# Performance work log

Hardware: AMD Instinct MI355X
Metric: run time of the kernel (lower is better)

The kernel has to match this reference:

```python
import jax, jax.numpy as jnp
import numpy as np

N = 65536       # n_nodes
E = 1048576     # n_edges (avg degree 16)
IDX = 256       # index_size
DIN = 512       # gcn_input_size
DH = 512        # gcn_hidden_size
DOUT = 128      # gcn_output_size
S = 256         # sample_size


def gcn_conv(h, W, b, src, dst, n):
    # PyG GCNConv: linear, add self-loops, symmetric deg^-1/2 normalization, scatter-add.
    h = h @ W
    loop = jnp.arange(n)
    s = jnp.concatenate([src, loop])
    d = jnp.concatenate([dst, loop])
    deg = jax.ops.segment_sum(jnp.ones(s.shape[0], h.dtype), d, num_segments=n)
    inv_sqrt = jax.lax.rsqrt(deg)  # deg >= 1 due to self-loops
    norm = inv_sqrt[s] * inv_sqrt[d]
    out = jax.ops.segment_sum(h[s] * norm[:, None], d, num_segments=n)
    return out + b


def _lin_init(k, fan_in, shape):
    bound = 1.0 / np.sqrt(fan_in)
    return jax.random.uniform(k, shape, jnp.float32, -bound, bound)


def setup_inputs() -> dict:
    key = jax.random.key(0)
    ks = jax.random.split(key, 14)
    x = jax.random.normal(ks[0], (N, IDX + 768), jnp.float32)
    edge_index = jax.random.randint(ks[1], (2, E), 0, N, dtype=jnp.int64)
    return {
        "x": x,
        "W_t1": _lin_init(ks[2], IDX, (IDX, DIN)),
        "b_t1": _lin_init(ks[3], IDX, (DIN,)),
        "W_t2": _lin_init(ks[4], 768, (768, DIN)),
        "b_t2": _lin_init(ks[5], 768, (DIN,)),
        "W1": _lin_init(ks[6], DIN, (DIN, DH)),
        "b1": _lin_init(ks[7], DIN, (DH,)),
        "W2": _lin_init(ks[8], DH, (DH, DOUT)),
        "b2": _lin_init(ks[9], DH, (DOUT,)),
        "matrix": jax.random.normal(ks[10], (DOUT, DOUT), jnp.float32),
        "lin_w": _lin_init(ks[11], 1, (2,)),   # nn.Linear(1, 2) weight, squeezed
        "lin_b": _lin_init(ks[12], 1, (2,)),
        "edge_index": edge_index,
    }


def reference(x, W_t1, b_t1, W_t2, b_t2, W1, b1, W2, b2, matrix, lin_w, lin_b, edge_index):
    src, dst = edge_index[0], edge_index[1]
    # dual-input linear fusion
    h = x[:, :IDX] @ W_t1 + b_t1 + x[:, IDX:] @ W_t2 + b_t2
    h = gcn_conv(h, W1, b1, src, dst, N)
    h = jax.nn.relu(h)  # dropout is identity in eval mode
    h = gcn_conv(h, W2, b2, src, dst, N)
    # per-sample bilinear score, batched over chunks
    e = h.reshape(N // S, S, DOUT)
    scores = jnp.einsum('bid,de,bje->bij', e, matrix, e)  # [B, S, S]
    out = scores[..., None] * lin_w + lin_b               # Linear(1, 2)
    return out.reshape(-1, 2)
```

## Files before the change

### kernel.cpp

```cpp
#include <hip/hip_runtime.h>
#include <stdint.h>

#define NN 65536

typedef __attribute__((ext_vector_type(8))) short bf16x8;
typedef __attribute__((ext_vector_type(4))) float f32x4;

__device__ __forceinline__ unsigned short f2bf(float f) {
    unsigned u = __float_as_uint(f);
    u += 0x7fffu + ((u >> 16) & 1u);
    return (unsigned short)(u >> 16);
}
__device__ __forceinline__ float bf2f(unsigned short h) { return __uint_as_float(((unsigned)h) << 16); }
__device__ __forceinline__ float blo(unsigned u) { return __uint_as_float(u << 16); }
__device__ __forceinline__ float bhi(unsigned u) { return __uint_as_float(u & 0xffff0000u); }
__device__ __forceinline__ unsigned pack2(float a, float b) {
    return ((unsigned)f2bf(b) << 16) | (unsigned)f2bf(a);
}
__device__ __forceinline__ unsigned trunc2(float x, float y) {
    return __builtin_amdgcn_perm(__float_as_uint(y), __float_as_uint(x), 0x07060302u);
}

__device__ __forceinline__ void gl_lds16(const void* g, void* l) {
    __builtin_amdgcn_global_load_lds((const __attribute__((address_space(1))) void*)g,
                                     (__attribute__((address_space(3))) void*)l, 16, 0, 0);
}

__global__ void prep_pack(const float* Wt1, const float* Wt2, const float* W1,
                          const float* W2, const float* Mtx,
                          unsigned short* Wcat, unsigned short* W1T,
                          unsigned short* W2T, unsigned short* MTh, unsigned short* MTl) {
    int i = blockIdx.x * 256 + threadIdx.x;
    if (i < 524288) {
        int k = i >> 9, j = i & 511;
        float v = (k < 256) ? Wt1[k * 512 + j] : Wt2[(k - 256) * 512 + j];
        Wcat[i] = f2bf(v);
    } else if (i < 786432) {
        int t = i - 524288; int n = t >> 9, j = t & 511;
        W1T[t] = f2bf(W1[j * 512 + n]);
    } else if (i < 851968) {
        int t = i - 786432; int n = t >> 9, j = t & 511;
        W2T[t] = f2bf(W2[j * 128 + n]);
    } else if (i < 868352) {
        int t = i - 851968; int d = t >> 7, e = t & 127;
        float m = Mtx[e * 128 + d];
        unsigned short h = f2bf(m);
        MTh[t] = h; MTl[t] = f2bf(m - bf2f(h));
    }
}

__global__ void cbias_k(const float* bt1, const float* bt2, const float* W1, float* c) {
    __shared__ float sm[256];
    int t = threadIdx.x;
    int n = blockIdx.x * 32 + (t & 31);
    int jp = t >> 5;
    float acc = 0.f;
    for (int j = jp * 64; j < jp * 64 + 64; j++)
        acc += (bt1[j] + bt2[j]) * W1[j * 512 + n];
    sm[t] = acc;
    __syncthreads();
    if (t < 32) {
        float a = 0.f;
#pragma unroll
        for (int p = 0; p < 8; p++) a += sm[p * 32 + t];
        c[blockIdx.x * 32 + t] = a;
    }
}

__global__ void count_k(const int* dst, int* cnt, int E) {
    int e = blockIdx.x * 256 + threadIdx.x;
    if (e < E) atomicAdd(&cnt[dst[e]], 1);
}
__global__ void red_k(const int* cnt, int* bsum) {
    __shared__ int sm[256];
    int tid = threadIdx.x;
    sm[tid] = cnt[blockIdx.x * 256 + tid];
    __syncthreads();
    for (int s = 128; s > 0; s >>= 1) {
        if (tid < s) sm[tid] += sm[tid + s];
        __syncthreads();
    }
    if (tid == 0) bsum[blockIdx.x] = sm[0];
}
__global__ void scanb_k(const int* bsum, int* boff) {
    __shared__ int sm[256];
    int tid = threadIdx.x;
    int v0 = bsum[tid];
    sm[tid] = v0;
    __syncthreads();
    for (int s = 1; s < 256; s <<= 1) {
        int t = sm[tid];
        if (tid >= s) t += sm[tid - s];
        __syncthreads();
        sm[tid] = t;
        __syncthreads();
    }
    boff[tid] = sm[tid] - v0;
}
__global__ void scanf_k(const int* cnt, const int* boff, int* rowptr, int* cursor, float* invs) {
    __shared__ int sm[256];
    int tid = threadIdx.x;
    int i = blockIdx.x * 256 + tid;
    int v = cnt[i];
    sm[tid] = v;
    __syncthreads();
    for (int s = 1; s < 256; s <<= 1) {
        int t = sm[tid];
        if (tid >= s) t += sm[tid - s];
        __syncthreads();
        sm[tid] = t;
        __syncthreads();
    }
    int incl = sm[tid];
    int base = boff[blockIdx.x];
    int excl = base + incl - v;
    rowptr[i] = excl;
    cursor[i] = excl;
    invs[i] = rsqrtf((float)(v + 1));
    if (i == NN - 1) rowptr[NN] = base + incl;
}
__global__ void fill_k(const int* src, const int* dst, int* cursor, int* colv, int E) {
    int e = blockIdx.x * 256 + threadIdx.x;
    if (e < E) {
        int d = dst[e];
        int p = atomicAdd(&cursor[d], 1);
        colv[p] = src[e];
    }
}

__global__ __launch_bounds__(256, 2) void gemm_bt(const unsigned short* A, const unsigned short* BT,
                                                  unsigned short* C, const float* bias,
                                                  int M, int N, int K) {
    __shared__ __align__(16) unsigned short sA[128 * 32];
    __shared__ __align__(16) unsigned short sB[128 * 32];
    int tid = threadIdx.x, wave = tid >> 6, lane = tid & 63;
    int bm = blockIdx.y * 128, bn = blockIdx.x * 128;
    int wm = (wave >> 1) * 64, wn = (wave & 1) * 64;
    f32x4 acc[4][4];
#pragma unroll
    for (int i = 0; i < 4; i++)
#pragma unroll
        for (int j = 0; j < 4; j++) acc[i][j] = (f32x4){0.f, 0.f, 0.f, 0.f};
    int sr = wave * 32 + (lane >> 2);
    int sc = (lane & 3) * 8;
    const int fr = lane & 15;
    const int fk = (lane >> 4) * 8;
    for (int k0 = 0; k0 < K; k0 += 32) {
        const unsigned short* ga = A + (size_t)(bm + sr) * K + k0 + sc;
        gl_lds16(ga, &sA[sr * 32 + sc]);
        gl_lds16(ga + (size_t)16 * K, &sA[(sr + 16) * 32 + sc]);
        const unsigned short* gb = BT + (size_t)(bn + sr) * K + k0 + sc;
        gl_lds16(gb, &sB[sr * 32 + sc]);
        gl_lds16(gb + (size_t)16 * K, &sB[(sr + 16) * 32 + sc]);
        __syncthreads();
        bf16x8 af[4], bfr[4];
#pragma unroll
        for (int i = 0; i < 4; i++) af[i] = *(const bf16x8*)&sA[(wm + i * 16 + fr) * 32 + fk];
#pragma unroll
        for (int j = 0; j < 4; j++) bfr[j] = *(const bf16x8*)&sB[(wn + j * 16 + fr) * 32 + fk];
#pragma unroll
        for (int i = 0; i < 4; i++)
#pragma unroll
            for (int j = 0; j < 4; j++)
                acc[i][j] = __builtin_amdgcn_mfma_f32_16x16x32_bf16(af[i], bfr[j], acc[i][j], 0, 0, 0);
        __syncthreads();
    }
    int rq = (lane >> 4) * 4;
#pragma unroll
    for (int i = 0; i < 4; i++)
#pragma unroll
        for (int j = 0; j < 4; j++) {
            int col = bn + wn + j * 16 + fr;
            float bb = bias ? bias[col] : 0.f;
#pragma unroll
            for (int r = 0; r < 4; r++) {
                int row = bm + wm + i * 16 + rq + r;
                C[(size_t)row * N + col] = f2bf(acc[i][j][r] + bb);
            }
        }
}

__global__ __launch_bounds__(256, 2) void gemm_f32a(const float* A, const unsigned short* BT,
                                                    unsigned short* C, const float* bias) {
    const int K = 1024, N = 512;
    __shared__ __align__(16) float sAf[128 * 32];
    __shared__ __align__(16) unsigned short sB[128 * 32];
    int tid = threadIdx.x, wave = tid >> 6, lane = tid & 63;
    int b = blockIdx.x;
    int xcd = b & 7, jn = (b >> 3) & 3, tt = b >> 5;
    int bm = (tt * 8 + xcd) * 128, bn = jn * 128;
    int wm = (wave >> 1) * 64, wn = (wave & 1) * 64;
    f32x4 acc[4][4];
#pragma unroll
    for (int i = 0; i < 4; i++)
#pragma unroll
        for (int j = 0; j < 4; j++) acc[i][j] = (f32x4){0.f, 0.f, 0.f, 0.f};
    int sr = wave * 32 + (lane >> 2);
    int sc = (lane & 3) * 8;
    int arow = lane >> 3;
    int achk = (lane & 7) ^ arow;
    const int fr = lane & 15;
    const int fk = (lane >> 4) * 8;
    const float* Abase = A + (size_t)(bm + wave * 32 + arow) * K + achk * 4;
    const unsigned short* Bbase = BT + (size_t)(bn + sr) * K + sc;
    for (int k0 = 0; k0 < K; k0 += 32) {
#pragma unroll
        for (int i = 0; i < 4; i++)
            gl_lds16(Abase + (size_t)(8 * i) * K + k0, &sAf[(wave * 32 + i * 8) * 32]);
        gl_lds16(Bbase + k0, &sB[sr * 32 + sc]);
        gl_lds16(Bbase + (size_t)16 * K + k0, &sB[(sr + 16) * 32 + sc]);
        __syncthreads();
        bf16x8 af[4], bfr[4];
#pragma unroll
        for (int i = 0; i < 4; i++) {
            int r = wm + i * 16 + fr;
            int s = r & 7;
            int c0 = fk >> 2;
            float4 fa = *(const float4*)&sAf[r * 32 + ((c0 ^ s) << 2)];
            float4 fb = *(const float4*)&sAf[r * 32 + (((c0 + 1) ^ s) << 2)];
            union { unsigned u[4]; bf16x8 v; } t;
            t.u[0] = trunc2(fa.x, fa.y);
            t.u[1] = trunc2(fa.z, fa.w);
            t.u[2] = trunc2(fb.x, fb.y);
            t.u[3] = trunc2(fb.z, fb.w);
            af[i] = t.v;
        }
#pragma unroll
        for (int j = 0; j < 4; j++) bfr[j] = *(const bf16x8*)&sB[(wn + j * 16 + fr) * 32 + fk];
#pragma unroll
        for (int i = 0; i < 4; i++)
#pragma unroll
            for (int j = 0; j < 4; j++)
                acc[i][j] = __builtin_amdgcn_mfma_f32_16x16x32_bf16(af[i], bfr[j], acc[i][j], 0, 0, 0);
        __syncthreads();
    }
    int rq = (lane >> 4) * 4;
#pragma unroll
    for (int i = 0; i < 4; i++)
#pragma unroll
        for (int j = 0; j < 4; j++) {
            int col = bn + wn + j * 16 + fr;
            float bb = bias[col];
#pragma unroll
            for (int r = 0; r < 4; r++) {
                int row = bm + wm + i * 16 + rq + r;
                C[(size_t)row * N + col] = f2bf(acc[i][j][r] + bb);
            }
        }
}

__global__ __launch_bounds__(256, 2) void gemm_T(const unsigned short* h2h, const unsigned short* h2l,
                                                 const unsigned short* MTh, const unsigned short* MTl,
                                                 unsigned short* Th, unsigned short* Tl) {
    __shared__ __align__(16) unsigned short sA[128 * 32];
    __shared__ __align__(16) unsigned short sB[128 * 32];
    int tid = threadIdx.x, wave = tid >> 6, lane = tid & 63;
    int bm = blockIdx.x * 128;
    int wm = (wave >> 1) * 64, wn = (wave & 1) * 64;
    f32x4 acc[4][4];
#pragma unroll
    for (int i = 0; i < 4; i++)
#pragma unroll
        for (int j = 0; j < 4; j++) acc[i][j] = (f32x4){0.f, 0.f, 0.f, 0.f};
    int sr = wave * 32 + (lane >> 2);
    int sc = (lane & 3) * 8;
    const int fr = lane & 15;
    const int fk = (lane >> 4) * 8;
    const unsigned short* APs[3] = {h2h, h2h, h2l};
    const unsigned short* BPs[3] = {MTh, MTl, MTh};
    for (int it = 0; it < 12; it++) {
        int ph = it >> 2, k0 = (it & 3) * 32;
        const unsigned short* ga = APs[ph] + (size_t)(bm + sr) * 128 + k0 + sc;
        gl_lds16(ga, &sA[sr * 32 + sc]);
        gl_lds16(ga + 16 * 128, &sA[(sr + 16) * 32 + sc]);
        const unsigned short* gb = BPs[ph] + (size_t)sr * 128 + k0 + sc;
        gl_lds16(gb, &sB[sr * 32 + sc]);
        gl_lds16(gb + 16 * 128, &sB[(sr + 16) * 32 + sc]);
        __syncthreads();
        bf16x8 af[4], bfr[4];
#pragma unroll
        for (int i = 0; i < 4; i++) af[i] = *(const bf16x8*)&sA[(wm + i * 16 + fr) * 32 + fk];
#pragma unroll
        for (int j = 0; j < 4; j++) bfr[j] = *(const bf16x8*)&sB[(wn + j * 16 + fr) * 32 + fk];
#pragma unroll
        for (int i = 0; i < 4; i++)
#pragma unroll
            for (int j = 0; j < 4; j++)
                acc[i][j] = __builtin_amdgcn_mfma_f32_16x16x32_bf16(af[i], bfr[j], acc[i][j], 0, 0, 0);
        __syncthreads();
    }
    int rq = (lane >> 4) * 4;
#pragma unroll
    for (int i = 0; i < 4; i++)
#pragma unroll
        for (int j = 0; j < 4; j++) {
            int col = wn + j * 16 + fr;
#pragma unroll
            for (int r = 0; r < 4; r++) {
                int row = bm + wm + i * 16 + rq + r;
                float v = acc[i][j][r];
                unsigned short h = f2bf(v);
                Th[(size_t)row * 128 + col] = h;
                Tl[(size_t)row * 128 + col] = f2bf(v - bf2f(h));
            }
        }
}

__global__ __launch_bounds__(256) void agg512(const unsigned short* t, const int* rowptr,
                                              const int* colv, const float* invs,
                                              const float* bias, unsigned short* outp) {
    int wave = threadIdx.x >> 6, lane = threadIdx.x & 63;
    int node = blockIdx.x * 4 + wave;
    int d0 = lane * 8;
    float acc[8] = {0.f, 0.f, 0.f, 0.f, 0.f, 0.f, 0.f, 0.f};
    int r0 = rowptr[node], r1 = rowptr[node + 1];
    int e = r0;
    for (; e + 4 <= r1; e += 4) {
        int s0 = colv[e], s1 = colv[e + 1], s2 = colv[e + 2], s3 = colv[e + 3];
        float w0 = invs[s0], w1 = invs[s1], w2 = invs[s2], w3 = invs[s3];
        uint4 v0 = *(const uint4*)&t[(size_t)s0 * 512 + d0];
        uint4 v1 = *(const uint4*)&t[(size_t)s1 * 512 + d0];
        uint4 v2 = *(const uint4*)&t[(size_t)s2 * 512 + d0];
        uint4 v3 = *(const uint4*)&t[(size_t)s3 * 512 + d0];
        acc[0] += w0 * blo(v0.x) + w1 * blo(v1.x) + w2 * blo(v2.x) + w3 * blo(v3.x);
        acc[1] += w0 * bhi(v0.x) + w1 * bhi(v1.x) + w2 * bhi(v2.x) + w3 * bhi(v3.x);
        acc[2] += w0 * blo(v0.y) + w1 * blo(v1.y) + w2 * blo(v2.y) + w3 * blo(v3.y);
        acc[3] += w0 * bhi(v0.y) + w1 * bhi(v1.y) + w2 * bhi(v2.y) + w3 * bhi(v3.y);
        acc[4] += w0 * blo(v0.z) + w1 * blo(v1.z) + w2 * blo(v2.z) + w3 * blo(v3.z);
        acc[5] += w0 * bhi(v0.z) + w1 * bhi(v1.z) + w2 * bhi(v2.z) + w3 * bhi(v3.z);
        acc[6] += w0 * blo(v0.w) + w1 * blo(v1.w) + w2 * blo(v2.w) + w3 * blo(v3.w);
        acc[7] += w0 * bhi(v0.w) + w1 * bhi(v1.w) + w2 * bhi(v2.w) + w3 * bhi(v3.w);
    }
    for (; e < r1; e++) {
        int s = colv[e];
        float ws = invs[s];
        uint4 v = *(const uint4*)&t[(size_t)s * 512 + d0];
        acc[0] += ws * blo(v.x); acc[1] += ws * bhi(v.x);
        acc[2] += ws * blo(v.y); acc[3] += ws * bhi(v.y);
        acc[4] += ws * blo(v.z); acc[5] += ws * bhi(v.z);
        acc[6] += ws * blo(v.w); acc[7] += ws * bhi(v.w);
    }
    float wd = invs[node], wdd = wd * wd;
    uint4 sv = *(const uint4*)&t[(size_t)node * 512 + d0];
    float sf[8] = {blo(sv.x), bhi(sv.x), blo(sv.y), bhi(sv.y), blo(sv.z), bhi(sv.z), blo(sv.w), bhi(sv.w)};
    float o[8];
#pragma unroll
    for (int k = 0; k < 8; k++) {
        float v = acc[k] * wd + sf[k] * wdd + bias[d0 + k];
        o[k] = v > 0.f ? v : 0.f;
    }
    uint4 pv;
    pv.x = pack2(o[0], o[1]); pv.y = pack2(o[2], o[3]);
    pv.z = pack2(o[4], o[5]); pv.w = pack2(o[6], o[7]);
    *(uint4*)&outp[(size_t)node * 512 + d0] = pv;
}

__global__ __launch_bounds__(256) void agg128(const unsigned short* u, const int* rowptr,
                                              const int* colv, const float* invs,
                                              const float* bias, unsigned short* h2h, unsigned short* h2l) {
    int wave = threadIdx.x >> 6, lane = threadIdx.x & 63;
    int node = blockIdx.x * 4 + wave;
    int q = lane >> 4, ql = lane & 15;
    int d0 = ql * 8;
    float acc[8] = {0.f, 0.f, 0.f, 0.f, 0.f, 0.f, 0.f, 0.f};
    int r0 = rowptr[node], r1 = rowptr[node + 1];
    for (int e = r0 + q; e < r1; e += 4) {
        int s = colv[e];
        float ws = invs[s];
        uint4 v = *(const uint4*)&u[(size_t)s * 128 + d0];
        acc[0] += ws * blo(v.x); acc[1] += ws * bhi(v.x);
        acc[2] += ws * blo(v.y); acc[3] += ws * bhi(v.y);
        acc[4] += ws * blo(v.z); acc[5] += ws * bhi(v.z);
        acc[6] += ws * blo(v.w); acc[7] += ws * bhi(v.w);
    }
#pragma unroll
    for (int k = 0; k < 8; k++) {
        acc[k] += __shfl_xor(acc[k], 16);
        acc[k] += __shfl_xor(acc[k], 32);
    }
    float wd = invs[node], wdd = wd * wd;
    uint4 sv = *(const uint4*)&u[(size_t)node * 128 + d0];
    float sf[8] = {blo(sv.x), bhi(sv.x), blo(sv.y), bhi(sv.y), blo(sv.z), bhi(sv.z), blo(sv.w), bhi(sv.w)};
    unsigned short hh[8], hl[8];
#pragma unroll
    for (int k = 0; k < 8; k++) {
        float v = acc[k] * wd + sf[k] * wdd + bias[d0 + k];
        hh[k] = f2bf(v);
        hl[k] = f2bf(v - bf2f(hh[k]));
    }
    if (q == 0) {
        uint4 ph, pl;
        ph.x = ((unsigned)hh[1] << 16) | hh[0]; ph.y = ((unsigned)hh[3] << 16) | hh[2];
        ph.z = ((unsigned)hh[5] << 16) | hh[4]; ph.w = ((unsigned)hh[7] << 16) | hh[6];
        pl.x = ((unsigned)hl[1] << 16) | hl[0]; pl.y = ((unsigned)hl[3] << 16) | hl[2];
        pl.z = ((unsigned)hl[5] << 16) | hl[4]; pl.w = ((unsigned)hl[7] << 16) | hl[6];
        *(uint4*)&h2h[(size_t)node * 128 + d0] = ph;
        *(uint4*)&h2l[(size_t)node * 128 + d0] = pl;
    }
}

__global__ __launch_bounds__(256, 2) void bilinear_k(const unsigned short* Th, const unsigned short* Tl,
                                                     const unsigned short* Eh, const float* lin_w,
                                                     const float* lin_b, float* outp) {
    int tid = threadIdx.x, wave = tid >> 6, lane = tid & 63;
    int b = blockIdx.x >> 1, half = blockIdx.x & 1;
    int fr = lane & 15, q = lane >> 4;
    int irow0 = b * 256 + half * 128 + wave * 32;
    bf16x8 Ah[2][4], Al[2][4];
#pragma unroll
    for (int it = 0; it < 2; it++)
#pragma unroll
        for (int kk = 0; kk < 4; kk++) {
            size_t off = (size_t)(irow0 + it * 16 + fr) * 128 + kk * 32 + q * 8;
            Ah[it][kk] = *(const bf16x8*)&Th[off];
            Al[it][kk] = *(const bf16x8*)&Tl[off];
        }
    float w0 = lin_w[0], w1 = lin_w[1], c0 = lin_b[0], c1 = lin_b[1];
    for (int jt = 0; jt < 16; jt++) {
        bf16x8 Bf[4];
#pragma unroll
        for (int kk = 0; kk < 4; kk++)
            Bf[kk] = *(const bf16x8*)&Eh[(size_t)(b * 256 + jt * 16 + fr) * 128 + kk * 32 + q * 8];
#pragma unroll
        for (int it = 0; it < 2; it++) {
            f32x4 acc = (f32x4){0.f, 0.f, 0.f, 0.f};
#pragma unroll
            for (int kk = 0; kk < 4; kk++) {
                acc = __builtin_amdgcn_mfma_f32_16x16x32_bf16(Ah[it][kk], Bf[kk], acc, 0, 0, 0);
                acc = __builtin_amdgcn_mfma_f32_16x16x32_bf16(Al[it][kk], Bf[kk], acc, 0, 0, 0);
            }
#pragma unroll
            for (int r = 0; r < 4; r++) {
                int iloc = half * 128 + wave * 32 + it * 16 + q * 4 + r;
                int jloc = jt * 16 + fr;
                size_t o = ((size_t)b * 65536 + (size_t)iloc * 256 + jloc) * 2;
                float s = acc[r];
                float2 ov;
                ov.x = fmaf(s, w0, c0);
                ov.y = fmaf(s, w1, c1);
                *(float2*)&outp[o] = ov;
            }
        }
    }
}

extern "C" void kernel_launch(void* const* d_in, const int* in_sizes, int n_in,
                              void* d_out, int out_size, void* d_ws, size_t ws_size,
                              hipStream_t stream) {
    const float* x   = (const float*)d_in[0];
    const float* Wt1 = (const float*)d_in[1];
    const float* bt1 = (const float*)d_in[2];
    const float* Wt2 = (const float*)d_in[3];
    const float* bt2 = (const float*)d_in[4];
    const float* W1  = (const float*)d_in[5];
    const float* b1  = (const float*)d_in[6];
    const float* W2  = (const float*)d_in[7];
    const float* b2  = (const float*)d_in[8];
    const float* Mtx = (const float*)d_in[9];
    const float* lw  = (const float*)d_in[10];
    const float* lb  = (const float*)d_in[11];
    const int*   ei  = (const int*)d_in[12];
    int E = in_sizes[12] / 2;
    const int* srcp = ei;
    const int* dstp = ei + E;

    unsigned char* p = (unsigned char*)d_ws;
    size_t off = 0;
    auto alloc = [&](size_t bytes) -> void* {
        void* r = p + off;
        off = (off + bytes + 255) & ~(size_t)255;
        return r;
    };
    int*   cnt    = (int*)alloc((size_t)NN * 4);
    int*   rowptr = (int*)alloc(((size_t)NN + 1) * 4);
    int*   cursor = (int*)alloc((size_t)NN * 4);
    float* invs   = (float*)alloc((size_t)NN * 4);
    int*   bsum   = (int*)alloc(256 * 4);
    int*   boff   = (int*)alloc(256 * 4);
    int*   colv   = (int*)alloc((size_t)E * 4);
    unsigned short* Wcat   = (unsigned short*)alloc(524288 * 2);
    unsigned short* W1T    = (unsigned short*)alloc(262144 * 2);
    unsigned short* W2T    = (unsigned short*)alloc(65536 * 2);
    unsigned short* MTh    = (unsigned short*)alloc(16384 * 2);
    unsigned short* MTl    = (unsigned short*)alloc(16384 * 2);
    float*          cbias  = (float*)alloc(512 * 4);
    unsigned short* WcombT = (unsigned short*)alloc(524288 * 2);
    unsigned short* t1     = (unsigned short*)alloc((size_t)NN * 512 * 2);
    unsigned short* h1     = (unsigned short*)alloc((size_t)NN * 512 * 2);
    unsigned short* uu     = (unsigned short*)alloc((size_t)NN * 128 * 2);
    unsigned short* Th  = t1;
    unsigned short* Tl  = t1 + (size_t)NN * 128;
    unsigned short* h2h = h1;
    unsigned short* h2l = h1 + (size_t)NN * 128;

    hipMemsetAsync(cnt, 0, (size_t)NN * 4, stream);
    prep_pack<<<3392, 256, 0, stream>>>(Wt1, Wt2, W1, W2, Mtx, Wcat, W1T, W2T, MTh, MTl);
    cbias_k<<<16, 256, 0, stream>>>(bt1, bt2, W1, cbias);
    count_k<<<(E + 255) / 256, 256, 0, stream>>>(dstp, cnt, E);
    red_k<<<256, 256, 0, stream>>>(cnt, bsum);
    scanb_k<<<1, 256, 0, stream>>>(bsum, boff);
    scanf_k<<<256, 256, 0, stream>>>(cnt, boff, rowptr, cursor, invs);
    fill_k<<<(E + 255) / 256, 256, 0, stream>>>(srcp, dstp, cursor, colv, E);
    gemm_bt<<<dim3(8, 4), 256, 0, stream>>>(W1T, Wcat, WcombT, nullptr, 512, 1024, 512);
    gemm_f32a<<<2048, 256, 0, stream>>>(x, WcombT, t1, cbias);
    agg512<<<NN / 4, 256, 0, stream>>>(t1, rowptr, colv, invs, b1, h1);
    gemm_bt<<<dim3(1, 512), 256, 0, stream>>>(h1, W2T, uu, nullptr, NN, 128, 512);
    agg128<<<NN / 4, 256, 0, stream>>>(uu, rowptr, colv, invs, b2, h2h, h2l);
    gemm_T<<<512, 256, 0, stream>>>(h2h, h2l, MTh, MTl, Th, Tl);
    bilinear_k<<<512, 256, 0, stream>>>(Th, Tl, h2h, lw, lb, (float*)d_out);
}
```

Before: 916.2 us.

## Pre-convert x to bf16 in chunks and use a bf16-input GEMM

The fused first GEMM used to stream fp32 x into LDS and truncate it to bf16 inside the inner loop. Now a separate kernel converts x to bf16 with round-to-nearest in two half-size chunks, reusing the h1 buffer as scratch, and a pure-bf16 GEMM runs on each chunk with higher occupancy (launch bounds 4). This halves GEMM A-operand traffic and LDS footprint and removes the conversion ALU work from the inner loop. In exchange it adds an extra read and write pass over x through HBM, plus extra launches.

```diff
diff --git a/kernel.cpp b/kernel.cpp
--- a/kernel.cpp
+++ b/kernel.cpp
@@ -16,9 +16,6 @@
 __device__ __forceinline__ float bhi(unsigned u) { return __uint_as_float(u & 0xffff0000u); }
 __device__ __forceinline__ unsigned pack2(float a, float b) {
     return ((unsigned)f2bf(b) << 16) | (unsigned)f2bf(a);
-}
-__device__ __forceinline__ unsigned trunc2(float x, float y) {
-    return __builtin_amdgcn_perm(__float_as_uint(y), __float_as_uint(x), 0x07060302u);
 }
 
 __device__ __forceinline__ void gl_lds16(const void* g, void* l) {
@@ -128,6 +125,21 @@
     }
 }
 
+__global__ void convx_k(const float* x, unsigned short* xb) {
+    int t = blockIdx.x * 256 + threadIdx.x;
+    for (int c = t; c < 2097152; c += 524288) {
+        const float4* s = (const float4*)(x + (size_t)c * 16);
+        float4 a = s[0], b = s[1], d = s[2], e = s[3];
+        uint4 o0, o1;
+        o0.x = pack2(a.x, a.y); o0.y = pack2(a.z, a.w);
+        o0.z = pack2(b.x, b.y); o0.w = pack2(b.z, b.w);
+        o1.x = pack2(d.x, d.y); o1.y = pack2(d.z, d.w);
+        o1.z = pack2(e.x, e.y); o1.w = pack2(e.z, e.w);
+        uint4* dst = (uint4*)(xb + (size_t)c * 16);
+        dst[0] = o0; dst[1] = o1;
+    }
+}
+
 __global__ __launch_bounds__(256, 2) void gemm_bt(const unsigned short* A, const unsigned short* BT,
                                                   unsigned short* C, const float* bias,
                                                   int M, int N, int K) {
@@ -180,10 +192,10 @@
         }
 }
 
-__global__ __launch_bounds__(256, 2) void gemm_f32a(const float* A, const unsigned short* BT,
-                                                    unsigned short* C, const float* bias) {
+__global__ __launch_bounds__(256, 4) void gemm_xb(const unsigned short* A, const unsigned short* BT,
+                                                  unsigned short* C, const float* bias) {
     const int K = 1024, N = 512;
-    __shared__ __align__(16) float sAf[128 * 32];
+    __shared__ __align__(16) unsigned short sA[128 * 32];
     __shared__ __align__(16) unsigned short sB[128 * 32];
     int tid = threadIdx.x, wave = tid >> 6, lane = tid & 63;
     int b = blockIdx.x;
@@ -197,34 +209,19 @@
         for (int j = 0; j < 4; j++) acc[i][j] = (f32x4){0.f, 0.f, 0.f, 0.f};
     int sr = wave * 32 + (lane >> 2);
     int sc = (lane & 3) * 8;
-    int arow = lane >> 3;
-    int achk = (lane & 7) ^ arow;
     const int fr = lane & 15;
     const int fk = (lane >> 4) * 8;
-    const float* Abase = A + (size_t)(bm + wave * 32 + arow) * K + achk * 4;
-    const unsigned short* Bbase = BT + (size_t)(bn + sr) * K + sc;
+    const unsigned short* ga = A + (size_t)(bm + sr) * K + sc;
+    const unsigned short* gb = BT + (size_t)(bn + sr) * K + sc;
     for (int k0 = 0; k0 < K; k0 += 32) {
-#pragma unroll
-        for (int i = 0; i < 4; i++)
-            gl_lds16(Abase + (size_t)(8 * i) * K + k0, &sAf[(wave * 32 + i * 8) * 32]);
-        gl_lds16(Bbase + k0, &sB[sr * 32 + sc]);
-        gl_lds16(Bbase + (size_t)16 * K + k0, &sB[(sr + 16) * 32 + sc]);
+        gl_lds16(ga + k0, &sA[sr * 32 + sc]);
+        gl_lds16(ga + (size_t)16 * K + k0, &sA[(sr + 16) * 32 + sc]);
+        gl_lds16(gb + k0, &sB[sr * 32 + sc]);
+        gl_lds16(gb + (size_t)16 * K + k0, &sB[(sr + 16) * 32 + sc]);
         __syncthreads();
         bf16x8 af[4], bfr[4];
 #pragma unroll
-        for (int i = 0; i < 4; i++) {
-            int r = wm + i * 16 + fr;
-            int s = r & 7;
-            int c0 = fk >> 2;
-            float4 fa = *(const float4*)&sAf[r * 32 + ((c0 ^ s) << 2)];
-            float4 fb = *(const float4*)&sAf[r * 32 + (((c0 + 1) ^ s) << 2)];
-            union { unsigned u[4]; bf16x8 v; } t;
-            t.u[0] = trunc2(fa.x, fa.y);
-            t.u[1] = trunc2(fa.z, fa.w);
-            t.u[2] = trunc2(fb.x, fb.y);
-            t.u[3] = trunc2(fb.z, fb.w);
-            af[i] = t.v;
-        }
+        for (int i = 0; i < 4; i++) af[i] = *(const bf16x8*)&sA[(wm + i * 16 + fr) * 32 + fk];
 #pragma unroll
         for (int j = 0; j < 4; j++) bfr[j] = *(const bf16x8*)&sB[(wn + j * 16 + fr) * 32 + fk];
 #pragma unroll
@@ -492,6 +489,7 @@
     unsigned short* Tl  = t1 + (size_t)NN * 128;
     unsigned short* h2h = h1;
     unsigned short* h2l = h1 + (size_t)NN * 128;
+    unsigned short* xb  = h1;
 
     hipMemsetAsync(cnt, 0, (size_t)NN * 4, stream);
     prep_pack<<<3392, 256, 0, stream>>>(Wt1, Wt2, W1, W2, Mtx, Wcat, W1T, W2T, MTh, MTl);
@@ -502,7 +500,10 @@
     scanf_k<<<256, 256, 0, stream>>>(cnt, boff, rowptr, cursor, invs);
     fill_k<<<(E + 255) / 256, 256, 0, stream>>>(srcp, dstp, cursor, colv, E);
     gemm_bt<<<dim3(8, 4), 256, 0, stream>>>(W1T, Wcat, WcombT, nullptr, 512, 1024, 512);
-    gemm_f32a<<<2048, 256, 0, stream>>>(x, WcombT, t1, cbias);
+    for (int ch = 0; ch < 2; ch++) {
+        convx_k<<<2048, 256, 0, stream>>>(x + (size_t)ch * 32768 * 1024, xb);
+        gemm_xb<<<1024, 256, 0, stream>>>(xb, WcombT, t1 + (size_t)ch * 32768 * 512, cbias);
+    }
     agg512<<<NN / 4, 256, 0, stream>>>(t1, rowptr, colv, invs, b1, h1);
     gemm_bt<<<dim3(1, 512), 256, 0, stream>>>(h1, W2T, uu, nullptr, NN, 128, 512);
     agg128<<<NN / 4, 256, 0, stream>>>(uu, rowptr, colv, invs, b2, h2h, h2l);
```

After: 943.7 us. 1.03x slower.

## Fold source-node normalization into GEMM epilogues and unroll aggregation gathers deeper

Applied to the files above, without the earlier changes.

The per-source deg^-1/2 scale now happens in the GEMM epilogues that produce t1 and uu, so the aggregation kernels no longer gather invs[src] per edge. The self-loop term is folded into the same sum, and a single multiply by the destination scale is applied at the end. agg512 now issues eight gathers per iteration and agg128 two per lane, which raises memory-level parallelism. Pre-scaling before bf16 rounding slightly changes the numerics, and the larger unroll adds register pressure.

```diff
diff --git a/kernel.cpp b/kernel.cpp
--- a/kernel.cpp
+++ b/kernel.cpp
@@ -130,6 +130,7 @@
 
 __global__ __launch_bounds__(256, 2) void gemm_bt(const unsigned short* A, const unsigned short* BT,
                                                   unsigned short* C, const float* bias,
+                                                  const float* rs,
                                                   int M, int N, int K) {
     __shared__ __align__(16) unsigned short sA[128 * 32];
     __shared__ __align__(16) unsigned short sB[128 * 32];
@@ -175,13 +176,15 @@
 #pragma unroll
             for (int r = 0; r < 4; r++) {
                 int row = bm + wm + i * 16 + rq + r;
-                C[(size_t)row * N + col] = f2bf(acc[i][j][r] + bb);
+                float scale = rs ? rs[row] : 1.f;
+                C[(size_t)row * N + col] = f2bf((acc[i][j][r] + bb) * scale);
             }
         }
 }
 
 __global__ __launch_bounds__(256, 2) void gemm_f32a(const float* A, const unsigned short* BT,
-                                                    unsigned short* C, const float* bias) {
+                                                    unsigned short* C, const float* bias,
+                                                    const float* rs) {
     const int K = 1024, N = 512;
     __shared__ __align__(16) float sAf[128 * 32];
     __shared__ __align__(16) unsigned short sB[128 * 32];
@@ -244,7 +247,7 @@
 #pragma unroll
             for (int r = 0; r < 4; r++) {
                 int row = bm + wm + i * 16 + rq + r;
-                C[(size_t)row * N + col] = f2bf(acc[i][j][r] + bb);
+                C[(size_t)row * N + col] = f2bf((acc[i][j][r] + bb) * rs[row]);
             }
         }
 }
@@ -314,39 +317,55 @@
     int d0 = lane * 8;
     float acc[8] = {0.f, 0.f, 0.f, 0.f, 0.f, 0.f, 0.f, 0.f};
     int r0 = rowptr[node], r1 = rowptr[node + 1];
+    uint4 sv = *(const uint4*)&t[(size_t)node * 512 + d0];
+    float wd = invs[node];
     int e = r0;
-    for (; e + 4 <= r1; e += 4) {
-        int s0 = colv[e], s1 = colv[e + 1], s2 = colv[e + 2], s3 = colv[e + 3];
-        float w0 = invs[s0], w1 = invs[s1], w2 = invs[s2], w3 = invs[s3];
-        uint4 v0 = *(const uint4*)&t[(size_t)s0 * 512 + d0];
-        uint4 v1 = *(const uint4*)&t[(size_t)s1 * 512 + d0];
-        uint4 v2 = *(const uint4*)&t[(size_t)s2 * 512 + d0];
-        uint4 v3 = *(const uint4*)&t[(size_t)s3 * 512 + d0];
-        acc[0] += w0 * blo(v0.x) + w1 * blo(v1.x) + w2 * blo(v2.x) + w3 * blo(v3.x);
-        acc[1] += w0 * bhi(v0.x) + w1 * bhi(v1.x) + w2 * bhi(v2.x) + w3 * bhi(v3.x);
-        acc[2] += w0 * blo(v0.y) + w1 * blo(v1.y) + w2 * blo(v2.y) + w3 * blo(v3.y);
-        acc[3] += w0 * bhi(v0.y) + w1 * bhi(v1.y) + w2 * bhi(v2.y) + w3 * bhi(v3.y);
-        acc[4] += w0 * blo(v0.z) + w1 * blo(v1.z) + w2 * blo(v2.z) + w3 * blo(v3.z);
-        acc[5] += w0 * bhi(v0.z) + w1 * bhi(v1.z) + w2 * bhi(v2.z) + w3 * bhi(v3.z);
-        acc[6] += w0 * blo(v0.w) + w1 * blo(v1.w) + w2 * blo(v2.w) + w3 * blo(v3.w);
-        acc[7] += w0 * bhi(v0.w) + w1 * bhi(v1.w) + w2 * bhi(v2.w) + w3 * bhi(v3.w);
+    for (; e + 8 <= r1; e += 8) {
+        int s[8];
+#pragma unroll
+        for (int c = 0; c < 8; c++) s[c] = colv[e + c];
+        uint4 v[8];
+#pragma unroll
+        for (int c = 0; c < 8; c++) v[c] = *(const uint4*)&t[(size_t)s[c] * 512 + d0];
+#pragma unroll
+        for (int c = 0; c < 8; c++) {
+            acc[0] += blo(v[c].x); acc[1] += bhi(v[c].x);
+            acc[2] += blo(v[c].y); acc[3] += bhi(v[c].y);
+            acc[4] += blo(v[c].z); acc[5] += bhi(v[c].z);
+            acc[6] += blo(v[c].w); acc[7] += bhi(v[c].w);
+        }
+    }
+    if (e + 4 <= r1) {
+        int s[4];
+#pragma unroll
+        for (int c = 0; c < 4; c++) s[c] = colv[e + c];
+        uint4 v[4];
+#pragma unroll
+        for (int c = 0; c < 4; c++) v[c] = *(const uint4*)&t[(size_t)s[c] * 512 + d0];
+#pragma unroll
+        for (int c = 0; c < 4; c++) {
+            acc[0] += blo(v[c].x); acc[1] += bhi(v[c].x);
+            acc[2] += blo(v[c].y); acc[3] += bhi(v[c].y);
+            acc[4] += blo(v[c].z); acc[5] += bhi(v[c].z);
+            acc[6] += blo(v[c].w); acc[7] += bhi(v[c].w);
+        }
+        e += 4;
     }
     for (; e < r1; e++) {
-        int s = colv[e];
-        float ws = invs[s];
-        uint4 v = *(const uint4*)&t[(size_t)s * 512 + d0];
-        acc[0] += ws * blo(v.x); acc[1] += ws * bhi(v.x);
-        acc[2] += ws * blo(v.y); acc[3] += ws * bhi(v.y);
-        acc[4] += ws * blo(v.z); acc[5] += ws * bhi(v.z);
-        acc[6] += ws * blo(v.w); acc[7] += ws * bhi(v.w);
-    }
-    float wd = invs[node], wdd = wd * wd;
-    uint4 sv = *(const uint4*)&t[(size_t)node * 512 + d0];
-    float sf[8] = {blo(sv.x), bhi(sv.x), blo(sv.y), bhi(sv.y), blo(sv.z), bhi(sv.z), blo(sv.w), bhi(sv.w)};
+        uint4 v = *(const uint4*)&t[(size_t)colv[e] * 512 + d0];
+        acc[0] += blo(v.x); acc[1] += bhi(v.x);
+        acc[2] += blo(v.y); acc[3] += bhi(v.y);
+        acc[4] += blo(v.z); acc[5] += bhi(v.z);
+        acc[6] += blo(v.w); acc[7] += bhi(v.w);
+    }
+    acc[0] += blo(sv.x); acc[1] += bhi(sv.x);
+    acc[2] += blo(sv.y); acc[3] += bhi(sv.y);
+    acc[4] += blo(sv.z); acc[5] += bhi(sv.z);
+    acc[6] += blo(sv.w); acc[7] += bhi(sv.w);
     float o[8];
 #pragma unroll
     for (int k = 0; k < 8; k++) {
-        float v = acc[k] * wd + sf[k] * wdd + bias[d0 + k];
+        float v = acc[k] * wd + bias[d0 + k];
         o[k] = v > 0.f ? v : 0.f;
     }
     uint4 pv;
@@ -364,27 +383,35 @@
     int d0 = ql * 8;
     float acc[8] = {0.f, 0.f, 0.f, 0.f, 0.f, 0.f, 0.f, 0.f};
     int r0 = rowptr[node], r1 = rowptr[node + 1];
-    for (int e = r0 + q; e < r1; e += 4) {
-        int s = colv[e];
-        float ws = invs[s];
-        uint4 v = *(const uint4*)&u[(size_t)s * 128 + d0];
-        acc[0] += ws * blo(v.x); acc[1] += ws * bhi(v.x);
-        acc[2] += ws * blo(v.y); acc[3] += ws * bhi(v.y);
-        acc[4] += ws * blo(v.z); acc[5] += ws * bhi(v.z);
-        acc[6] += ws * blo(v.w); acc[7] += ws * bhi(v.w);
+    uint4 sv = *(const uint4*)&u[(size_t)node * 128 + d0];
+    float wd = invs[node];
+    int e = r0 + q;
+    for (; e + 4 < r1; e += 8) {
+        int s0 = colv[e], s1 = colv[e + 4];
+        uint4 v0 = *(const uint4*)&u[(size_t)s0 * 128 + d0];
+        uint4 v1 = *(const uint4*)&u[(size_t)s1 * 128 + d0];
+        acc[0] += blo(v0.x) + blo(v1.x); acc[1] += bhi(v0.x) + bhi(v1.x);
+        acc[2] += blo(v0.y) + blo(v1.y); acc[3] += bhi(v0.y) + bhi(v1.y);
+        acc[4] += blo(v0.z) + blo(v1.z); acc[5] += bhi(v0.z) + bhi(v1.z);
+        acc[6] += blo(v0.w) + blo(v1.w); acc[7] += bhi(v0.w) + bhi(v1.w);
+    }
+    if (e < r1) {
+        uint4 v = *(const uint4*)&u[(size_t)colv[e] * 128 + d0];
+        acc[0] += blo(v.x); acc[1] += bhi(v.x);
+        acc[2] += blo(v.y); acc[3] += bhi(v.y);
+        acc[4] += blo(v.z); acc[5] += bhi(v.z);
+        acc[6] += blo(v.w); acc[7] += bhi(v.w);
     }
 #pragma unroll
     for (int k = 0; k < 8; k++) {
         acc[k] += __shfl_xor(acc[k], 16);
         acc[k] += __shfl_xor(acc[k], 32);
     }
-    float wd = invs[node], wdd = wd * wd;
-    uint4 sv = *(const uint4*)&u[(size_t)node * 128 + d0];
     float sf[8] = {blo(sv.x), bhi(sv.x), blo(sv.y), bhi(sv.y), blo(sv.z), bhi(sv.z), blo(sv.w), bhi(sv.w)};
     unsigned short hh[8], hl[8];
 #pragma unroll
     for (int k = 0; k < 8; k++) {
-        float v = acc[k] * wd + sf[k] * wdd + bias[d0 + k];
+        float v = (acc[k] + sf[k]) * wd + bias[d0 + k];
         hh[k] = f2bf(v);
         hl[k] = f2bf(v - bf2f(hh[k]));
     }
@@ -501,10 +528,10 @@
     scanb_k<<<1, 256, 0, stream>>>(bsum, boff);
     scanf_k<<<256, 256, 0, stream>>>(cnt, boff, rowptr, cursor, invs);
     fill_k<<<(E + 255) / 256, 256, 0, stream>>>(srcp, dstp, cursor, colv, E);
-    gemm_bt<<<dim3(8, 4), 256, 0, stream>>>(W1T, Wcat, WcombT, nullptr, 512, 1024, 512);
-    gemm_f32a<<<2048, 256, 0, stream>>>(x, WcombT, t1, cbias);
+    gemm_bt<<<dim3(8, 4), 256, 0, stream>>>(W1T, Wcat, WcombT, nullptr, nullptr, 512, 1024, 512);
+    gemm_f32a<<<2048, 256, 0, stream>>>(x, WcombT, t1, cbias, invs);
     agg512<<<NN / 4, 256, 0, stream>>>(t1, rowptr, colv, invs, b1, h1);
-    gemm_bt<<<dim3(1, 512), 256, 0, stream>>>(h1, W2T, uu, nullptr, NN, 128, 512);
+    gemm_bt<<<dim3(1, 512), 256, 0, stream>>>(h1, W2T, uu, nullptr, invs, NN, 128, 512);
     agg128<<<NN / 4, 256, 0, stream>>>(uu, rowptr, colv, invs, b2, h2h, h2l);
     gemm_T<<<512, 256, 0, stream>>>(h2h, h2l, MTh, MTl, Th, Tl);
     bilinear_k<<<512, 256, 0, stream>>>(Th, Tl, h2h, lw, lb, (float*)d_out);
```

Result: no change. 912.8 us (-0.4%).
